# Performance work log

Hardware: AMD Instinct MI355X
Metric: run time of the kernel (lower is better)

The kernel has to match this reference:

```python
import jax, jax.numpy as jnp
import numpy as np

N = 50000      # nodes
E = 1600000    # edges
IN = 128       # in_features
OUT = 64       # out_features
H = 2          # heads
ALPHA = 0.2    # LeakyReLU negative slope


def setup_inputs() -> dict:
    key = jax.random.key(0)
    k1, k2, k3, k4 = jax.random.split(key, 4)
    x = jax.random.normal(k1, (N, IN), dtype=jnp.float32)
    edge_index = jax.random.randint(k2, (2, E), 0, N, dtype=jnp.int32)
    # xavier-uniform-ish scaled params
    W = jax.random.normal(k3, (H, IN, OUT), dtype=jnp.float32) / np.float32(np.sqrt(IN))
    a = jax.random.normal(k4, (H, 2 * OUT, 1), dtype=jnp.float32) * np.float32(0.1)
    return {"x": x, "W": W, "a": a, "edge_index": edge_index}


def reference(x, W, a, edge_index):
    src = edge_index[0]
    dst = edge_index[1]
    # per-head linear transform: [N, H, O]
    Wh = jnp.einsum('ni,hio->nho', x, W)
    # split attention vector: a @ [Wh_i || Wh_j] == Wh_i@a_i + Wh_j@a_j
    a_i = a[:, :OUT, 0]   # [H, O]
    a_j = a[:, OUT:, 0]   # [H, O]
    s_i = jnp.einsum('nho,ho->nh', Wh, a_i)   # [N, H]
    s_j = jnp.einsum('nho,ho->nh', Wh, a_j)   # [N, H]
    # per-edge attention logits, LeakyReLU
    e = jax.nn.leaky_relu(s_i[src] + s_j[dst], negative_slope=ALPHA)  # [E, H]
    # faithful to source: GLOBAL softmax over all edges (dim=0) per head
    attn = jax.nn.softmax(e, axis=0)  # [E, H]
    # dropout with rate 0.0 -> identity (eval mode)
    msg = attn[:, :, None] * Wh[dst]  # [E, H, O]
    h = jax.ops.segment_sum(msg, dst, num_segments=N)  # [N, H, O]
    # concat heads along feature dim
    return h.reshape(N, H * OUT)
```

## Files before the change

### kernel.cpp

```cpp
#include <hip/hip_runtime.h>

#define NN 50000
#define EE 1600000
#define INF 128
#define OUTF 64
#define NH 2
#define ALPHA 0.2f

#define RNG 16
#define NPR (NN / RNG)
#define NBB 64
#define EPB (EE / NBB)
#define BCAP 2048
#define NSPREP 391
#define NWPREP 64
#define NBNODE 391
#define HCH 16
#define SPB (NBB / HCH)

typedef __attribute__((ext_vector_type(8))) short s16x8;
typedef __attribute__((ext_vector_type(4))) float f32x4;

__device__ __forceinline__ unsigned short bf16_rne(float f) {
    union { float f; unsigned u; } v; v.f = f;
    unsigned r = v.u + 0x7FFFu + ((v.u >> 16) & 1u);
    return (unsigned short)(r >> 16);
}
__device__ __forceinline__ float bf16_val(unsigned short h) {
    union { unsigned u; float f; } v; v.u = ((unsigned)h) << 16;
    return v.f;
}
__device__ __forceinline__ void split8(const float4 a, const float4 b,
                                       s16x8& hi, s16x8& lo) {
    const float p[8] = {a.x, a.y, a.z, a.w, b.x, b.y, b.z, b.w};
    #pragma unroll
    for (int j = 0; j < 8; ++j) {
        const unsigned short h = bf16_rne(p[j]);
        hi[j] = (short)h;
        lo[j] = (short)bf16_rne(p[j] - bf16_val(h));
    }
}


__global__ __launch_bounds__(256)
void gat_prep(const float* __restrict__ x, const float* __restrict__ Wg,
              const float* __restrict__ av, const int* __restrict__ ei,
              float* __restrict__ si, float* __restrict__ sj,
              unsigned short* __restrict__ Wf, unsigned* __restrict__ buckets,
              int* __restrict__ counts, float* __restrict__ Z)
{
    __shared__ float4 u4[128];
    __shared__ int cnt[16];
    const int tid = threadIdx.x;

    if (blockIdx.x >= NSPREP + NBB) {
        const int idx = (blockIdx.x - (NSPREP + NBB)) * 256 + tid;
        if (idx < 2) Z[idx] = 0.0f;
        const int h = idx >> 13;
        const int k = (idx >> 6) & 127;
        const int o = idx & 63;
        const float w = Wg[idx];
        const unsigned short hi = bf16_rne(w);
        const unsigned short lo = bf16_rne(w - bf16_val(hi));
        const int n  = h * 64 + o;
        const int nt = n >> 4;
        const int ks = k >> 5;
        const int kk = k & 31;
        const int ln = (kk >> 3) * 16 + (n & 15);
        const int pos = ((nt * 4 + ks) * 64 + ln) * 8 + (kk & 7);
        Wf[pos] = hi;
        Wf[16384 + pos] = lo;
        return;
    }

    if (blockIdx.x >= NSPREP) {
        const int bid = blockIdx.x - NSPREP;
        if (tid < 16) cnt[tid] = 0;
        __syncthreads();
        const int e0 = bid * EPB;
        for (int i = tid; i < EPB / 4; i += 256) {
            const int4 s4 = *(const int4*)&ei[e0 + 4 * i];
            const int4 d4 = *(const int4*)&ei[EE + e0 + 4 * i];
            const int ss[4] = {s4.x, s4.y, s4.z, s4.w};
            const int dd[4] = {d4.x, d4.y, d4.z, d4.w};
            #pragma unroll
            for (int k = 0; k < 4; ++k) {
                const int r = dd[k] / NPR;
                const int rel = dd[k] - r * NPR;
                const int pos = atomicAdd(&cnt[r], 1);
                if (pos < BCAP)
                    buckets[(size_t)(r * NBB + bid) * BCAP + pos] =
                        (unsigned)ss[k] | ((unsigned)rel << 16);
            }
        }
        __syncthreads();
        if (tid < 16) counts[tid * NBB + bid] = min(cnt[tid], BCAP);
        return;
    }

    if (tid < 128) {
        const int k = tid;
        float u0 = 0.f, u1 = 0.f, u2 = 0.f, u3 = 0.f;
        #pragma unroll 4
        for (int o = 0; o < 64; o += 4) {
            const float4 w0 = *(const float4*)&Wg[k * 64 + o];
            const float4 w1 = *(const float4*)&Wg[8192 + k * 64 + o];
            const float4 ai0 = *(const float4*)&av[o];
            const float4 aj0 = *(const float4*)&av[64 + o];
            const float4 ai1 = *(const float4*)&av[128 + o];
            const float4 aj1 = *(const float4*)&av[192 + o];
            u0 += w0.x*ai0.x + w0.y*ai0.y + w0.z*ai0.z + w0.w*ai0.w;
            u1 += w0.x*aj0.x + w0.y*aj0.y + w0.z*aj0.z + w0.w*aj0.w;
            u2 += w1.x*ai1.x + w1.y*ai1.y + w1.z*ai1.z + w1.w*ai1.w;
            u3 += w1.x*aj1.x + w1.y*aj1.y + w1.z*aj1.z + w1.w*aj1.w;
        }
        u4[k] = make_float4(u0, u1, u2, u3);
    }
    __syncthreads();

    const int lane = tid & 63;
    const int wv = tid >> 6;
    const int lm = lane & 15;
    const int rsub = lane >> 4;

    #pragma unroll
    for (int p = 0; p < 8; ++p) {
        const int row = blockIdx.x * 128 + p * 16 + wv * 4 + rsub;
        const int rc = row < NN ? row : NN - 1;
        const float4 xa = *(const float4*)(x + (size_t)rc * INF + lm * 8);
        const float4 xb = *(const float4*)(x + (size_t)rc * INF + lm * 8 + 4);
        float s0 = 0.f, s1 = 0.f, s2 = 0.f, s3 = 0.f;
        const float xv[8] = {xa.x, xa.y, xa.z, xa.w, xb.x, xb.y, xb.z, xb.w};
        #pragma unroll
        for (int j = 0; j < 8; ++j) {
            const float4 u = u4[lm * 8 + j];
            s0 = fmaf(xv[j], u.x, s0);
            s1 = fmaf(xv[j], u.y, s1);
            s2 = fmaf(xv[j], u.z, s2);
            s3 = fmaf(xv[j], u.w, s3);
        }
        #pragma unroll
        for (int m = 1; m < 16; m <<= 1) {
            s0 += __shfl_xor(s0, m, 64);
            s1 += __shfl_xor(s1, m, 64);
            s2 += __shfl_xor(s2, m, 64);
            s3 += __shfl_xor(s3, m, 64);
        }
        if (lm == 0 && row < NN) {
            *(float2*)&si[2 * row] = make_float2(s0, s2);
            *(float2*)&sj[2 * row] = make_float2(s1, s3);
        }
    }
}

__global__ __launch_bounds__(512)
void gat_hist(const unsigned* __restrict__ buckets, const int* __restrict__ counts,
              const float* __restrict__ si, const float* __restrict__ sj,
              float* __restrict__ partial, float* __restrict__ Z)
{
    __shared__ float bins[NPR * 2];
    __shared__ float zr0[8], zr1[8];
    const int c = blockIdx.x;
    const int r = blockIdx.y;
    const int nlo = r * NPR;

    for (int i = threadIdx.x; i < NPR; i += 512)
        ((float2*)bins)[i] = make_float2(0.f, 0.f);
    __syncthreads();

    float z0 = 0.f, z1 = 0.f;
    #pragma unroll
    for (int bb = 0; bb < SPB; ++bb) {
        const int b = c * SPB + bb;
        const int n = counts[r * NBB + b];
        const uint4* seg4 = (const uint4*)(buckets + (size_t)(r * NBB + b) * BCAP);
        const int n4 = (n + 3) >> 2;
        for (int i = threadIdx.x; i < n4; i += 512) {
            const uint4 pk4 = seg4[i];
            const unsigned pks[4] = {pk4.x, pk4.y, pk4.z, pk4.w};
            #pragma unroll
            for (int j = 0; j < 4; ++j) {
                if (4 * i + j < n) {
                    const unsigned pk = pks[j];
                    const int s = (int)(pk & 0xFFFFu);
                    const int rel = (int)(pk >> 16);
                    const float2 vi = *(const float2*)&si[2 * s];
                    const float2 vj = *(const float2*)&sj[2 * (nlo + rel)];
                    float a0 = vi.x + vj.x; a0 = a0 > 0.f ? a0 : ALPHA * a0;
                    float a1 = vi.y + vj.y; a1 = a1 > 0.f ? a1 : ALPHA * a1;
                    const float w0 = expf(a0);
                    const float w1 = expf(a1);
                    atomicAdd(&bins[2 * rel], w0);
                    atomicAdd(&bins[2 * rel + 1], w1);
                    z0 += w0; z1 += w1;
                }
            }
        }
    }

    #pragma unroll
    for (int m = 1; m < 64; m <<= 1) {
        z0 += __shfl_xor(z0, m, 64);
        z1 += __shfl_xor(z1, m, 64);
    }
    const int wv = threadIdx.x >> 6;
    if ((threadIdx.x & 63) == 0) { zr0[wv] = z0; zr1[wv] = z1; }
    __syncthreads();
    if (threadIdx.x == 0) {
        float t0 = 0.f, t1 = 0.f;
        #pragma unroll
        for (int i = 0; i < 8; ++i) { t0 += zr0[i]; t1 += zr1[i]; }
        atomicAdd(&Z[0], t0);
        atomicAdd(&Z[1], t1);
    }

    float2* P = (float2*)(partial + (size_t)c * 100000 + nlo * 2);
    for (int i = threadIdx.x; i < NPR; i += 512)
        P[i] = ((const float2*)bins)[i];
}

__global__ __launch_bounds__(256)
void gat_node(const float* __restrict__ x, const unsigned short* __restrict__ Wf,
              const float* __restrict__ partial, const float* __restrict__ Z,
              float* __restrict__ out)
{
    __shared__ unsigned short WsL[32768];
    const int tid = threadIdx.x;
    const int lane = tid & 63;
    const int wv = tid >> 6;
    const int lm = lane & 15;
    const int quad = lane >> 4;

    {
        const float4* gsrc = (const float4*)Wf;
        float4* ldst = (float4*)WsL;
        #pragma unroll
        for (int i = 0; i < 16; ++i)
            ldst[i * 256 + tid] = gsrc[i * 256 + tid];
    }

    const float rz0 = 1.0f / Z[0];
    const float rz1 = 1.0f / Z[1];

    const int rowA0 = blockIdx.x * 128 + wv * 32 + lm;
    const int rowA1 = rowA0 + 16;
    const int rc0 = rowA0 < NN ? rowA0 : NN - 1;
    const int rc1 = rowA1 < NN ? rowA1 : NN - 1;
    const float* xp0 = x + (size_t)rc0 * INF + quad * 8;
    const float* xp1 = x + (size_t)rc1 * INF + quad * 8;

    f32x4 acc[2][8];
    #pragma unroll
    for (int mi = 0; mi < 2; ++mi)
        #pragma unroll
        for (int nt = 0; nt < 8; ++nt) acc[mi][nt] = (f32x4)0.0f;

    __syncthreads();

    #pragma unroll
    for (int ks = 0; ks < 4; ++ks) {
        s16x8 ah0, al0, ah1, al1;
        {
            const float4 u0 = *(const float4*)(xp0 + ks * 32);
            const float4 v0 = *(const float4*)(xp0 + ks * 32 + 4);
            split8(u0, v0, ah0, al0);
            const float4 u1 = *(const float4*)(xp1 + ks * 32);
            const float4 v1 = *(const float4*)(xp1 + ks * 32 + 4);
            split8(u1, v1, ah1, al1);
        }
        #pragma unroll
        for (int nt = 0; nt < 8; ++nt) {
            const s16x8 bh = *(const s16x8*)&WsL[((nt * 4 + ks) * 64 + lane) * 8];
            const s16x8 bl = *(const s16x8*)&WsL[16384 + ((nt * 4 + ks) * 64 + lane) * 8];
            acc[0][nt] = __builtin_amdgcn_mfma_f32_16x16x32_bf16(ah0, bh, acc[0][nt], 0, 0, 0);
            acc[0][nt] = __builtin_amdgcn_mfma_f32_16x16x32_bf16(ah0, bl, acc[0][nt], 0, 0, 0);
            acc[0][nt] = __builtin_amdgcn_mfma_f32_16x16x32_bf16(al0, bh, acc[0][nt], 0, 0, 0);
            acc[1][nt] = __builtin_amdgcn_mfma_f32_16x16x32_bf16(ah1, bh, acc[1][nt], 0, 0, 0);
            acc[1][nt] = __builtin_amdgcn_mfma_f32_16x16x32_bf16(ah1, bl, acc[1][nt], 0, 0, 0);
            acc[1][nt] = __builtin_amdgcn_mfma_f32_16x16x32_bf16(al1, bh, acc[1][nt], 0, 0, 0);
        }
    }

    #pragma unroll
    for (int mi = 0; mi < 2; ++mi) {
        const int rowb = blockIdx.x * 128 + wv * 32 + mi * 16 + quad * 4;
        #pragma unroll
        for (int r = 0; r < 4; ++r) {
            const int rr = rowb + r;
            const int rrc = rr < NN ? rr : NN - 1;
            float v0 = partial[(size_t)lm * 100000 + 2 * rrc];
            float v1 = partial[(size_t)lm * 100000 + 2 * rrc + 1];
            #pragma unroll
            for (int m = 1; m < 16; m <<= 1) {
                v0 += __shfl_xor(v0, m, 64);
                v1 += __shfl_xor(v1, m, 64);
            }
            const float sc0 = v0 * rz0;
            const float sc1 = v1 * rz1;
            if (rr < NN) {
                float* orow = out + (size_t)rr * (NH * OUTF) + lm;
                #pragma unroll
                for (int nt = 0; nt < 8; ++nt)
                    orow[nt * 16] = acc[mi][nt][r] * (nt < 4 ? sc0 : sc1);
            }
        }
    }
}

extern "C" void kernel_launch(void* const* d_in, const int* in_sizes, int n_in,
                              void* d_out, int out_size, void* d_ws, size_t ws_size,
                              hipStream_t stream)
{
    const float* x = (const float*)d_in[0];
    const float* W = (const float*)d_in[1];
    const float* a = (const float*)d_in[2];
    const int* ei = (const int*)d_in[3];
    float* out = (float*)d_out;
    float* ws = (float*)d_ws;

    float* si = ws;
    float* sj = ws + 100000;
    float* Z = ws + 200000;
    int* counts = (int*)(ws + 200016);
    unsigned short* Wf = (unsigned short*)(ws + 201056);
    unsigned* buckets = (unsigned*)(ws + 217472);
    float* partial = ws + 2314624;

    gat_prep<<<dim3(NSPREP + NBB + NWPREP), dim3(256), 0, stream>>>(
        x, W, a, ei, si, sj, Wf, buckets, counts, Z);

    gat_hist<<<dim3(HCH, RNG), dim3(512), 0, stream>>>(buckets, counts, si, sj,
                                                       partial, Z);

    gat_node<<<dim3(NBNODE), dim3(256), 0, stream>>>(x, Wf, partial, Z, out);
}
```

Before: 145.0 us.

## Replace bucketed LDS histogram with direct global atomic scatter of edge weights

Drops the destination-range bucketing pass and the LDS-bin histogram kernel with its per-chunk partial buffers. A single edge kernel now reads the edge list directly, computes exp weights and atomically adds them into a global per-node sum. The node kernel then reads one float2 per row instead of reducing 16 partials. This cuts a pass over the edges and the bucket traffic, at the cost of 3.2M contended global float atomics and a zeroing loop moved into the prep kernel.

Result: slower. 290.3 us (+100.2%).

```diff
diff --git a/kernel.cpp b/kernel.cpp
--- a/kernel.cpp
+++ b/kernel.cpp
@@ -7,16 +7,10 @@
 #define NH 2
 #define ALPHA 0.2f
 
-#define RNG 16
-#define NPR (NN / RNG)
-#define NBB 64
-#define EPB (EE / NBB)
-#define BCAP 2048
 #define NSPREP 391
 #define NWPREP 64
 #define NBNODE 391
-#define HCH 16
-#define SPB (NBB / HCH)
+#define NEBLK 1024
 
 typedef __attribute__((ext_vector_type(8))) short s16x8;
 typedef __attribute__((ext_vector_type(4))) float f32x4;
@@ -44,18 +38,17 @@
 
 __global__ __launch_bounds__(256)
 void gat_prep(const float* __restrict__ x, const float* __restrict__ Wg,
-              const float* __restrict__ av, const int* __restrict__ ei,
+              const float* __restrict__ av,
               float* __restrict__ si, float* __restrict__ sj,
-              unsigned short* __restrict__ Wf, unsigned* __restrict__ buckets,
-              int* __restrict__ counts, float* __restrict__ Z)
+              unsigned short* __restrict__ Wf, float* __restrict__ azero)
 {
     __shared__ float4 u4[128];
-    __shared__ int cnt[16];
     const int tid = threadIdx.x;
 
-    if (blockIdx.x >= NSPREP + NBB) {
-        const int idx = (blockIdx.x - (NSPREP + NBB)) * 256 + tid;
-        if (idx < 2) Z[idx] = 0.0f;
+    if (blockIdx.x >= NSPREP) {
+        const int idx = (blockIdx.x - NSPREP) * 256 + tid;
+        for (int j = idx; j < 200002; j += NWPREP * 256)
+            azero[j] = 0.0f;
         const int h = idx >> 13;
         const int k = (idx >> 6) & 127;
         const int o = idx & 63;
@@ -73,31 +66,6 @@
         return;
     }
 
-    if (blockIdx.x >= NSPREP) {
-        const int bid = blockIdx.x - NSPREP;
-        if (tid < 16) cnt[tid] = 0;
-        __syncthreads();
-        const int e0 = bid * EPB;
-        for (int i = tid; i < EPB / 4; i += 256) {
-            const int4 s4 = *(const int4*)&ei[e0 + 4 * i];
-            const int4 d4 = *(const int4*)&ei[EE + e0 + 4 * i];
-            const int ss[4] = {s4.x, s4.y, s4.z, s4.w};
-            const int dd[4] = {d4.x, d4.y, d4.z, d4.w};
-            #pragma unroll
-            for (int k = 0; k < 4; ++k) {
-                const int r = dd[k] / NPR;
-                const int rel = dd[k] - r * NPR;
-                const int pos = atomicAdd(&cnt[r], 1);
-                if (pos < BCAP)
-                    buckets[(size_t)(r * NBB + bid) * BCAP + pos] =
-                        (unsigned)ss[k] | ((unsigned)rel << 16);
-            }
-        }
-        __syncthreads();
-        if (tid < 16) counts[tid * NBB + bid] = min(cnt[tid], BCAP);
-        return;
-    }
-
     if (tid < 128) {
         const int k = tid;
         float u0 = 0.f, u1 = 0.f, u2 = 0.f, u3 = 0.f;
@@ -153,48 +121,34 @@
     }
 }
 
-__global__ __launch_bounds__(512)
-void gat_hist(const unsigned* __restrict__ buckets, const int* __restrict__ counts,
+__global__ __launch_bounds__(256)
+void gat_edge(const int* __restrict__ ei,
               const float* __restrict__ si, const float* __restrict__ sj,
-              float* __restrict__ partial, float* __restrict__ Z)
-{
-    __shared__ float bins[NPR * 2];
-    __shared__ float zr0[8], zr1[8];
-    const int c = blockIdx.x;
-    const int r = blockIdx.y;
-    const int nlo = r * NPR;
-
-    for (int i = threadIdx.x; i < NPR; i += 512)
-        ((float2*)bins)[i] = make_float2(0.f, 0.f);
-    __syncthreads();
+              float* __restrict__ attnsum, float* __restrict__ Z)
+{
+    __shared__ float zr0[4], zr1[4];
+    const int gid = blockIdx.x * 256 + threadIdx.x;
+    const int gsz = gridDim.x * 256;
+    const int4* src4 = (const int4*)ei;
+    const int4* dst4 = (const int4*)(ei + EE);
 
     float z0 = 0.f, z1 = 0.f;
-    #pragma unroll
-    for (int bb = 0; bb < SPB; ++bb) {
-        const int b = c * SPB + bb;
-        const int n = counts[r * NBB + b];
-        const uint4* seg4 = (const uint4*)(buckets + (size_t)(r * NBB + b) * BCAP);
-        const int n4 = (n + 3) >> 2;
-        for (int i = threadIdx.x; i < n4; i += 512) {
-            const uint4 pk4 = seg4[i];
-            const unsigned pks[4] = {pk4.x, pk4.y, pk4.z, pk4.w};
-            #pragma unroll
-            for (int j = 0; j < 4; ++j) {
-                if (4 * i + j < n) {
-                    const unsigned pk = pks[j];
-                    const int s = (int)(pk & 0xFFFFu);
-                    const int rel = (int)(pk >> 16);
-                    const float2 vi = *(const float2*)&si[2 * s];
-                    const float2 vj = *(const float2*)&sj[2 * (nlo + rel)];
-                    float a0 = vi.x + vj.x; a0 = a0 > 0.f ? a0 : ALPHA * a0;
-                    float a1 = vi.y + vj.y; a1 = a1 > 0.f ? a1 : ALPHA * a1;
-                    const float w0 = expf(a0);
-                    const float w1 = expf(a1);
-                    atomicAdd(&bins[2 * rel], w0);
-                    atomicAdd(&bins[2 * rel + 1], w1);
-                    z0 += w0; z1 += w1;
-                }
-            }
+    for (int i = gid; i < EE / 4; i += gsz) {
+        const int4 s4 = src4[i];
+        const int4 d4 = dst4[i];
+        const int ss[4] = {s4.x, s4.y, s4.z, s4.w};
+        const int dd[4] = {d4.x, d4.y, d4.z, d4.w};
+        #pragma unroll
+        for (int k = 0; k < 4; ++k) {
+            const float2 vi = *(const float2*)&si[2 * ss[k]];
+            const float2 vj = *(const float2*)&sj[2 * dd[k]];
+            float a0 = vi.x + vj.x; a0 = a0 > 0.f ? a0 : ALPHA * a0;
+            float a1 = vi.y + vj.y; a1 = a1 > 0.f ? a1 : ALPHA * a1;
+            const float w0 = expf(a0);
+            const float w1 = expf(a1);
+            atomicAdd(&attnsum[2 * dd[k]], w0);
+            atomicAdd(&attnsum[2 * dd[k] + 1], w1);
+            z0 += w0; z1 += w1;
         }
     }
 
@@ -207,21 +161,16 @@
     if ((threadIdx.x & 63) == 0) { zr0[wv] = z0; zr1[wv] = z1; }
     __syncthreads();
     if (threadIdx.x == 0) {
-        float t0 = 0.f, t1 = 0.f;
-        #pragma unroll
-        for (int i = 0; i < 8; ++i) { t0 += zr0[i]; t1 += zr1[i]; }
+        const float t0 = zr0[0] + zr0[1] + zr0[2] + zr0[3];
+        const float t1 = zr1[0] + zr1[1] + zr1[2] + zr1[3];
         atomicAdd(&Z[0], t0);
         atomicAdd(&Z[1], t1);
     }
-
-    float2* P = (float2*)(partial + (size_t)c * 100000 + nlo * 2);
-    for (int i = threadIdx.x; i < NPR; i += 512)
-        P[i] = ((const float2*)bins)[i];
 }
 
 __global__ __launch_bounds__(256)
 void gat_node(const float* __restrict__ x, const unsigned short* __restrict__ Wf,
-              const float* __restrict__ partial, const float* __restrict__ Z,
+              const float* __restrict__ attnsum, const float* __restrict__ Z,
               float* __restrict__ out)
 {
     __shared__ unsigned short WsL[32768];
@@ -287,17 +236,10 @@
         #pragma unroll
         for (int r = 0; r < 4; ++r) {
             const int rr = rowb + r;
-            const int rrc = rr < NN ? rr : NN - 1;
-            float v0 = partial[(size_t)lm * 100000 + 2 * rrc];
-            float v1 = partial[(size_t)lm * 100000 + 2 * rrc + 1];
-            #pragma unroll
-            for (int m = 1; m < 16; m <<= 1) {
-                v0 += __shfl_xor(v0, m, 64);
-                v1 += __shfl_xor(v1, m, 64);
-            }
-            const float sc0 = v0 * rz0;
-            const float sc1 = v1 * rz1;
             if (rr < NN) {
+                const float2 as = *(const float2*)&attnsum[2 * rr];
+                const float sc0 = as.x * rz0;
+                const float sc1 = as.y * rz1;
                 float* orow = out + (size_t)rr * (NH * OUTF) + lm;
                 #pragma unroll
                 for (int nt = 0; nt < 8; ++nt)
@@ -320,17 +262,14 @@
 
     float* si = ws;
     float* sj = ws + 100000;
-    float* Z = ws + 200000;
-    int* counts = (int*)(ws + 200016);
-    unsigned short* Wf = (unsigned short*)(ws + 201056);
-    unsigned* buckets = (unsigned*)(ws + 217472);
-    float* partial = ws + 2314624;
-
-    gat_prep<<<dim3(NSPREP + NBB + NWPREP), dim3(256), 0, stream>>>(
-        x, W, a, ei, si, sj, Wf, buckets, counts, Z);
-
-    gat_hist<<<dim3(HCH, RNG), dim3(512), 0, stream>>>(buckets, counts, si, sj,
-                                                       partial, Z);
-
-    gat_node<<<dim3(NBNODE), dim3(256), 0, stream>>>(x, Wf, partial, Z, out);
-}
+    float* attnsum = ws + 200000;
+    float* Z = ws + 400000;
+    unsigned short* Wf = (unsigned short*)(ws + 400064);
+
+    gat_prep<<<dim3(NSPREP + NWPREP), dim3(256), 0, stream>>>(
+        x, W, a, si, sj, Wf, attnsum);
+
+    gat_edge<<<dim3(NEBLK), dim3(256), 0, stream>>>(ei, si, sj, attnsum, Z);
+
+    gat_node<<<dim3(NBNODE), dim3(256), 0, stream>>>(x, Wf, attnsum, Z, out);
+}
```
